# Kernel optimization log

Measured on AMD Instinct MI355X. Metric: run time of the kernel, lower is better.

## Reference

```python
import jax, jax.numpy as jnp
import numpy as np

B, T, N = 512, 1024, 50
ROOT_IDX, END_IDX = 0, 1
NEG_INF = -10000.0


def setup_inputs() -> dict:
    key = jax.random.key(0)
    k1, k2, k3, k4 = jax.random.split(key, 4)
    input_features = jax.random.normal(k1, (B, T, N), dtype=jnp.float32)
    # xavier_uniform on [N, N]: bound = sqrt(6 / (N + N))
    bound = float(np.sqrt(6.0 / (N + N)))
    log_transitions = jax.random.uniform(k2, (N, N), minval=-bound, maxval=bound, dtype=jnp.float32)
    log_transitions = log_transitions.at[:, ROOT_IDX].set(NEG_INF)
    log_transitions = log_transitions.at[END_IDX, :].set(NEG_INF)
    target_tags = jax.random.randint(k3, (B, T), 0, N).astype(jnp.int64)
    # contiguous prefix mask from random lengths in [T//2, T]
    lengths = jax.random.randint(k4, (B,), T // 2, T + 1)
    input_mask = (jnp.arange(T)[None, :] < lengths[:, None]).astype(jnp.int32)
    return {
        "input_features": input_features,
        "log_transitions": log_transitions,
        "target_tags": target_tags,
        "input_mask": input_mask,
    }


def _crf_nll(input_features, log_transitions, target_tags, input_mask):
    maskf = input_mask.astype(input_features.dtype)  # [B, T]

    # ---- forward belief propagation (log partition) ----
    alpha0 = log_transitions[ROOT_IDX, :][None, :] + input_features[:, 0, :]  # [B, N]
    feats_t = jnp.swapaxes(input_features, 0, 1)  # [T, B, N]
    mask_t = jnp.swapaxes(maskf, 0, 1)            # [T, B]

    def step(alpha, xs):
        feat, m = xs  # [B, N], [B]
        # next_tag_var[b, i, j] = alpha[b, i] + feat[b, j] + trans[i, j]
        nxt = alpha[:, :, None] + feat[:, None, :] + log_transitions[None, :, :]
        new = jax.nn.logsumexp(nxt, axis=1)  # [B, N]
        m = m[:, None]
        return new * m + alpha * (1.0 - m), None

    alpha, _ = jax.lax.scan(step, alpha0, (feats_t[1:], mask_t[1:]))
    log_z = jax.nn.logsumexp(alpha + log_transitions[:, END_IDX][None, :], axis=-1)  # [B]

    # ---- gold sequence score (vectorized over time) ----
    tags = target_tags  # [B, T]
    scores = log_transitions[ROOT_IDX, tags[:, 0]]  # [B]
    # per-position emission score of the gold tag
    emis = jnp.take_along_axis(input_features, tags[:, :, None], axis=2)[:, :, 0]  # [B, T]
    trans = log_transitions[tags[:, :-1], tags[:, 1:]]  # [B, T-1]
    scores = scores + jnp.sum(trans * maskf[:, 1:], axis=1) + jnp.sum(emis[:, :-1] * maskf[:, :-1], axis=1)
    last_idx = jnp.sum(input_mask, axis=1) - 1  # [B]
    last_tags = jnp.take_along_axis(tags, last_idx[:, None], axis=1)[:, 0]  # [B]
    last_emit = jnp.take_along_axis(input_features[:, -1, :], last_tags[:, None], axis=1)[:, 0]
    scores = scores + log_transitions[last_tags, END_IDX] + last_emit * maskf[:, -1]

    return log_z - scores  # negative log likelihood, [B]


def reference(input_features, log_transitions, target_tags, input_mask):
    return _crf_nll(input_features, log_transitions, target_tags, input_mask)
```

## Files before the change

### kernel.cpp

```cpp
#include <hip/hip_runtime.h>
#include <math.h>

#define BB 512
#define TT 1024
#define NS 50

typedef _Float16 half2_t __attribute__((ext_vector_type(2)));

static __device__ __forceinline__ half2_t pk_h2(float a, float b) {
    auto r = __builtin_amdgcn_cvt_pkrtz(a, b);
    return __builtin_bit_cast(half2_t, r);
}
static __device__ __forceinline__ float wave_sum_f(float v) {
    #pragma unroll
    for (int k = 32; k >= 1; k >>= 1) v += __shfl_xor(v, k, 64);
    return v;
}
static __device__ __forceinline__ int wave_sum_i(int v) {
    #pragma unroll
    for (int k = 32; k >= 1; k >>= 1) v += __shfl_xor(v, k, 64);
    return v;
}
#define FDOT(a, b, c) __builtin_amdgcn_fdot2((a), (b), (c), false)

__global__ __launch_bounds__(128, 1) void crf_nll_kernel(
    const float* __restrict__ feat,
    const float* __restrict__ trans,
    const int*   __restrict__ tags,
    const int*   __restrict__ mask,
    float* __restrict__ out)
{
    const int b    = blockIdx.x;
    const int tid  = threadIdx.x;
    const int w    = tid >> 6;
    const int lane = tid & 63;
    const int jj   = (lane < NS) ? lane : 0;

    __shared__ float sh_comb[64];
    __shared__ float sh_sc[2];
    __shared__ int   sh_Kb;

#define INIT_E(m) half2_t e##m; { \
        int r0 = w ? (jj * NS + 2*(m)) : ((2*(m)) * NS + jj); \
        int r1 = r0 + (w ? 1 : NS); \
        float x0 = __expf(trans[r0]); \
        float x1 = __expf(trans[r1]); \
        if (lane >= NS) { x0 = 0.f; x1 = 0.f; } \
        e##m = pk_h2(x0, x1); }
    INIT_E(0)  INIT_E(1)  INIT_E(2)  INIT_E(3)  INIT_E(4)
    INIT_E(5)  INIT_E(6)  INIT_E(7)  INIT_E(8)  INIT_E(9)
    INIT_E(10) INIT_E(11) INIT_E(12) INIT_E(13) INIT_E(14)
    INIT_E(15) INIT_E(16) INIT_E(17) INIT_E(18) INIT_E(19)
    INIT_E(20) INIT_E(21) INIT_E(22) INIT_E(23) INIT_E(24)
#undef INIT_E

    int cnt = 0;
    for (int t = lane; t < TT; t += 64) cnt += mask[b * TT + t];
    const int len = wave_sum_i(cnt);
    const int tm  = (len - 1) >> 1;
    const int nst = w ? (len - 1 - tm) : tm;

    const float* fb = feat + (size_t)b * TT * NS;

    float u;
    if (w == 0) u = (lane < NS) ? __expf(trans[jj] + fb[jj]) : 0.f;
    else        u = (lane < NS) ? __expf(trans[jj * NS + 1] + fb[(size_t)(len - 1) * NS + jj]) : 0.f;
    int K = 0, kp, rr;
    { int bb2 = __builtin_amdgcn_readlane(__float_as_int(u), 7);
      kp = ((bb2 >> 23) & 255) - 127; rr = (127 - kp) << 23; }

    auto step = [&](float eexp) {
        K += kp;
        float p = u * __int_as_float(rr);
        int pn_ = __builtin_amdgcn_update_dpp(
            __float_as_int(p), __float_as_int(p), 0xB1, 0xF, 0xF, true);
        float pnf = __int_as_float(pn_);
        half2_t pk = pk_h2(p, pnf);
        int pki = __builtin_bit_cast(int, pk);
        float s0 = 0.f, s1 = 0.f, s2 = 0.f, s3 = 0.f;
        float s4 = 0.f, s5 = 0.f, s6 = 0.f, s7 = 0.f;
#define RLF(m, acc) { int b_ = __builtin_amdgcn_readlane(pki, 2*(m)); \
        acc = FDOT(__builtin_bit_cast(half2_t, b_), e##m, acc); }
        RLF(0,  s0) RLF(1,  s1) RLF(2,  s2) RLF(3,  s3)
        RLF(4,  s4) RLF(5,  s5) RLF(6,  s6) RLF(7,  s7)
        RLF(8,  s0) RLF(9,  s1) RLF(10, s2) RLF(11, s3)
        RLF(12, s4) RLF(13, s5) RLF(14, s6) RLF(15, s7)
        RLF(16, s0) RLF(17, s1) RLF(18, s2) RLF(19, s3)
        RLF(20, s4) RLF(21, s5) RLF(22, s6) RLF(23, s7)
        RLF(24, s0)
#undef RLF
        float S = ((s0 + s1) + (s2 + s3)) + ((s4 + s5) + (s6 + s7));
        u = S * eexp;
        int bb2 = __builtin_amdgcn_readlane(__float_as_int(u), 7);
        kp = ((bb2 >> 23) & 255) - 127;
        rr = (127 - kp) << 23;
    };

    float q0, q1, q2, q3, q4, q5, q6, q7;
    {
        int t0 = w ? (len - 2) : 1;
        int st = w ? -1 : 1;
#define LD(qr, d) { int tl = t0 + st * (d); tl = (tl < 0) ? 0 : ((tl < TT) ? tl : TT - 1); \
                    qr = __expf(fb[(size_t)tl * NS + jj]); }
        LD(q0, 0) LD(q1, 1) LD(q2, 2) LD(q3, 3) LD(q4, 4) LD(q5, 5) LD(q6, 6) LD(q7, 7)
#undef LD
    }

#define PF_STEP(qr, d) { \
        float e_ = qr; \
        int kl = k + 8 + (d); \
        int tl = w ? (len - 2 - kl) : (1 + kl); \
        tl = (tl < 0) ? 0 : ((tl < TT) ? tl : TT - 1); \
        qr = __expf(fb[(size_t)tl * NS + jj]); \
        step(e_); }

    int k = 0;
    for (; k + 8 <= nst; k += 8) {
        PF_STEP(q0, 0) PF_STEP(q1, 1) PF_STEP(q2, 2) PF_STEP(q3, 3)
        PF_STEP(q4, 4) PF_STEP(q5, 5) PF_STEP(q6, 6) PF_STEP(q7, 7)
    }
#undef PF_STEP
    for (; k < nst; ++k) {
        int tl = w ? (len - 2 - k) : (1 + k);
        step(__expf(fb[(size_t)tl * NS + jj]));
    }

    if (w == 1) {
        sh_comb[lane] = u * __expf(-fb[(size_t)tm * NS + jj]);
        if (lane == 0) sh_Kb = K;
    }

    const int* tb = tags + (size_t)b * TT;
    float sc = 0.0f;
    for (int t2 = tid; t2 < len; t2 += 128) {
        int tg = tb[t2];
        sc += fb[(size_t)t2 * NS + tg];
        if (t2 >= 1) sc += trans[tb[t2 - 1] * NS + tg];
    }
    sc = wave_sum_f(sc);
    if (lane == 0) sh_sc[w] = sc;

    __syncthreads();

    if (w == 0) {
        float wv = u * sh_comb[lane];
        float W = wave_sum_f(wv);
        float log_z = __logf(W) + (float)(K + sh_Kb) * 0.6931471805599453f;
        if (lane == 0) {
            float sct = sh_sc[0] + sh_sc[1]
                      + trans[tb[0]]
                      + trans[tb[len - 1] * NS + 1];
            out[b] = log_z - sct;
        }
    }
}

extern "C" void kernel_launch(void* const* d_in, const int* in_sizes, int n_in,
                              void* d_out, int out_size, void* d_ws, size_t ws_size,
                              hipStream_t stream) {
    const float* feat  = (const float*)d_in[0];
    const float* trans = (const float*)d_in[1];
    const int*   tags  = (const int*)d_in[2];
    const int*   mask  = (const int*)d_in[3];
    float* out = (float*)d_out;
    crf_nll_kernel<<<dim3(BB), dim3(128), 0, stream>>>(feat, trans, tags, mask, out);
}
```

Measured before the change: 275.3 us.

## Batch 16 sequences per block with MFMA recurrence and producer-wave LDS staging

The forward recursion is rebuilt so each block handles 16 sequences and computes the 50x50 transition product with 16x16x32 f16 MFMA instead of per-lane readlane and fdot2 chains. Dedicated producer waves load emission rows, exponentiate them and stage them in a ring of LDS slots, synchronised with the consumer waves by barriers. The gold-path score moves into a separate kernel whose result goes through a workspace. The aim is to remove the serial scalar dependency per step and raise arithmetic density. The cost is an extra launch, block barriers on every group of four steps, a launch of only 32 blocks, and every sequence running to the batch's longest length.

```diff
diff --git a/kernel.cpp b/kernel.cpp
--- a/kernel.cpp
+++ b/kernel.cpp
@@ -4,153 +4,303 @@
 #define BB 512
 #define TT 1024
 #define NS 50
-
+#define SEQ 16
+#define LN2F 0.6931471805599453f
+
+typedef _Float16 f16x8 __attribute__((ext_vector_type(8)));
 typedef _Float16 half2_t __attribute__((ext_vector_type(2)));
-
-static __device__ __forceinline__ half2_t pk_h2(float a, float b) {
+typedef float f32x4 __attribute__((ext_vector_type(4)));
+
+#define MFMA16(A, B, C) __builtin_amdgcn_mfma_f32_16x16x32_f16((A), (B), (C), 0, 0, 0)
+
+static __device__ __forceinline__ int pack2(float a, float b) {
     auto r = __builtin_amdgcn_cvt_pkrtz(a, b);
-    return __builtin_bit_cast(half2_t, r);
+    return __builtin_bit_cast(int, r);
 }
-static __device__ __forceinline__ float wave_sum_f(float v) {
-    #pragma unroll
-    for (int k = 32; k >= 1; k >>= 1) v += __shfl_xor(v, k, 64);
-    return v;
-}
-static __device__ __forceinline__ int wave_sum_i(int v) {
-    #pragma unroll
-    for (int k = 32; k >= 1; k >>= 1) v += __shfl_xor(v, k, 64);
-    return v;
-}
-#define FDOT(a, b, c) __builtin_amdgcn_fdot2((a), (b), (c), false)
-
-__global__ __launch_bounds__(128, 1) void crf_nll_kernel(
+
+#define SLOT_F 924
+#define TILE_F 264
+#define T3_F   792
+#define DIR_F  (8 * SLOT_F)
+
+struct ES { f32x4 a, b, c; float x0, x1; };
+struct LS { f32x4 a, b, c, d; };
+
+__global__ __launch_bounds__(128, 1) void crf_score_kernel(
     const float* __restrict__ feat,
     const float* __restrict__ trans,
     const int*   __restrict__ tags,
     const int*   __restrict__ mask,
-    float* __restrict__ out)
+    float* __restrict__ ws)
 {
     const int b    = blockIdx.x;
     const int tid  = threadIdx.x;
     const int w    = tid >> 6;
     const int lane = tid & 63;
-    const int jj   = (lane < NS) ? lane : 0;
-
-    __shared__ float sh_comb[64];
     __shared__ float sh_sc[2];
-    __shared__ int   sh_Kb;
-
-#define INIT_E(m) half2_t e##m; { \
-        int r0 = w ? (jj * NS + 2*(m)) : ((2*(m)) * NS + jj); \
-        int r1 = r0 + (w ? 1 : NS); \
-        float x0 = __expf(trans[r0]); \
-        float x1 = __expf(trans[r1]); \
-        if (lane >= NS) { x0 = 0.f; x1 = 0.f; } \
-        e##m = pk_h2(x0, x1); }
-    INIT_E(0)  INIT_E(1)  INIT_E(2)  INIT_E(3)  INIT_E(4)
-    INIT_E(5)  INIT_E(6)  INIT_E(7)  INIT_E(8)  INIT_E(9)
-    INIT_E(10) INIT_E(11) INIT_E(12) INIT_E(13) INIT_E(14)
-    INIT_E(15) INIT_E(16) INIT_E(17) INIT_E(18) INIT_E(19)
-    INIT_E(20) INIT_E(21) INIT_E(22) INIT_E(23) INIT_E(24)
-#undef INIT_E
 
     int cnt = 0;
     for (int t = lane; t < TT; t += 64) cnt += mask[b * TT + t];
-    const int len = wave_sum_i(cnt);
-    const int tm  = (len - 1) >> 1;
-    const int nst = w ? (len - 1 - tm) : tm;
-
-    const float* fb = feat + (size_t)b * TT * NS;
-
-    float u;
-    if (w == 0) u = (lane < NS) ? __expf(trans[jj] + fb[jj]) : 0.f;
-    else        u = (lane < NS) ? __expf(trans[jj * NS + 1] + fb[(size_t)(len - 1) * NS + jj]) : 0.f;
-    int K = 0, kp, rr;
-    { int bb2 = __builtin_amdgcn_readlane(__float_as_int(u), 7);
-      kp = ((bb2 >> 23) & 255) - 127; rr = (127 - kp) << 23; }
-
-    auto step = [&](float eexp) {
-        K += kp;
-        float p = u * __int_as_float(rr);
-        int pn_ = __builtin_amdgcn_update_dpp(
-            __float_as_int(p), __float_as_int(p), 0xB1, 0xF, 0xF, true);
-        float pnf = __int_as_float(pn_);
-        half2_t pk = pk_h2(p, pnf);
-        int pki = __builtin_bit_cast(int, pk);
-        float s0 = 0.f, s1 = 0.f, s2 = 0.f, s3 = 0.f;
-        float s4 = 0.f, s5 = 0.f, s6 = 0.f, s7 = 0.f;
-#define RLF(m, acc) { int b_ = __builtin_amdgcn_readlane(pki, 2*(m)); \
-        acc = FDOT(__builtin_bit_cast(half2_t, b_), e##m, acc); }
-        RLF(0,  s0) RLF(1,  s1) RLF(2,  s2) RLF(3,  s3)
-        RLF(4,  s4) RLF(5,  s5) RLF(6,  s6) RLF(7,  s7)
-        RLF(8,  s0) RLF(9,  s1) RLF(10, s2) RLF(11, s3)
-        RLF(12, s4) RLF(13, s5) RLF(14, s6) RLF(15, s7)
-        RLF(16, s0) RLF(17, s1) RLF(18, s2) RLF(19, s3)
-        RLF(20, s4) RLF(21, s5) RLF(22, s6) RLF(23, s7)
-        RLF(24, s0)
-#undef RLF
-        float S = ((s0 + s1) + (s2 + s3)) + ((s4 + s5) + (s6 + s7));
-        u = S * eexp;
-        int bb2 = __builtin_amdgcn_readlane(__float_as_int(u), 7);
-        kp = ((bb2 >> 23) & 255) - 127;
-        rr = (127 - kp) << 23;
-    };
-
-    float q0, q1, q2, q3, q4, q5, q6, q7;
-    {
-        int t0 = w ? (len - 2) : 1;
-        int st = w ? -1 : 1;
-#define LD(qr, d) { int tl = t0 + st * (d); tl = (tl < 0) ? 0 : ((tl < TT) ? tl : TT - 1); \
-                    qr = __expf(fb[(size_t)tl * NS + jj]); }
-        LD(q0, 0) LD(q1, 1) LD(q2, 2) LD(q3, 3) LD(q4, 4) LD(q5, 5) LD(q6, 6) LD(q7, 7)
-#undef LD
-    }
-
-#define PF_STEP(qr, d) { \
-        float e_ = qr; \
-        int kl = k + 8 + (d); \
-        int tl = w ? (len - 2 - kl) : (1 + kl); \
-        tl = (tl < 0) ? 0 : ((tl < TT) ? tl : TT - 1); \
-        qr = __expf(fb[(size_t)tl * NS + jj]); \
-        step(e_); }
-
-    int k = 0;
-    for (; k + 8 <= nst; k += 8) {
-        PF_STEP(q0, 0) PF_STEP(q1, 1) PF_STEP(q2, 2) PF_STEP(q3, 3)
-        PF_STEP(q4, 4) PF_STEP(q5, 5) PF_STEP(q6, 6) PF_STEP(q7, 7)
-    }
-#undef PF_STEP
-    for (; k < nst; ++k) {
-        int tl = w ? (len - 2 - k) : (1 + k);
-        step(__expf(fb[(size_t)tl * NS + jj]));
-    }
-
-    if (w == 1) {
-        sh_comb[lane] = u * __expf(-fb[(size_t)tm * NS + jj]);
-        if (lane == 0) sh_Kb = K;
-    }
-
-    const int* tb = tags + (size_t)b * TT;
-    float sc = 0.0f;
+    #pragma unroll
+    for (int k = 32; k >= 1; k >>= 1) cnt += __shfl_xor(cnt, k, 64);
+    const int len = cnt;
+
+    const float* fbb = feat + (size_t)b * TT * NS;
+    const int*   tb  = tags + (size_t)b * TT;
+    float sc = 0.f;
     for (int t2 = tid; t2 < len; t2 += 128) {
         int tg = tb[t2];
-        sc += fb[(size_t)t2 * NS + tg];
+        sc += fbb[(size_t)t2 * NS + tg];
         if (t2 >= 1) sc += trans[tb[t2 - 1] * NS + tg];
     }
-    sc = wave_sum_f(sc);
+    #pragma unroll
+    for (int k = 32; k >= 1; k >>= 1) sc += __shfl_xor(sc, k, 64);
     if (lane == 0) sh_sc[w] = sc;
-
     __syncthreads();
-
-    if (w == 0) {
-        float wv = u * sh_comb[lane];
-        float W = wave_sum_f(wv);
-        float log_z = __logf(W) + (float)(K + sh_Kb) * 0.6931471805599453f;
-        if (lane == 0) {
-            float sct = sh_sc[0] + sh_sc[1]
-                      + trans[tb[0]]
-                      + trans[tb[len - 1] * NS + 1];
-            out[b] = log_z - sct;
+    if (tid == 0)
+        ws[b] = sh_sc[0] + sh_sc[1] + trans[tb[0]] + trans[tb[len - 1] * NS + 1];
+}
+
+__global__ __launch_bounds__(256, 1) void crf_main_kernel(
+    const float* __restrict__ feat,
+    const float* __restrict__ trans,
+    const int*   __restrict__ mask,
+    const float* __restrict__ score_ws,
+    float* __restrict__ out)
+{
+    const int tid  = threadIdx.x;
+    const int wv   = tid >> 6;
+    const int role = wv >> 1;
+    const int dir  = wv & 1;
+    const int l    = tid & 63;
+    const int c    = l & 15;
+    const int g    = l >> 4;
+    const int base = blockIdx.x * SEQ;
+
+    __shared__ float eL[2 * DIR_F];
+    __shared__ float comb[64][16];
+    __shared__ int   shK[16];
+
+    const float* fb = feat + (size_t)(base + c) * TT * NS;
+
+    int cnt = 0;
+    {
+        const int4* mp4 = (const int4*)(mask + (size_t)(base + c) * TT) + g * 64;
+        #pragma unroll 4
+        for (int i = 0; i < 64; ++i) { int4 m = mp4[i]; cnt += m.x + m.y + m.z + m.w; }
+    }
+    cnt += __shfl_xor(cnt, 16, 64);
+    cnt += __shfl_xor(cnt, 32, 64);
+    const int len   = cnt;
+    const int tm    = (len - 1) >> 1;
+    const int nst   = dir ? (len - 1 - tm) : tm;
+    const int lastk = nst - 1;
+
+    int bm = (tm > len - 1 - tm) ? tm : (len - 1 - tm);
+    #pragma unroll
+    for (int k = 1; k < 64; k <<= 1) { int o = __shfl_xor(bm, k, 64); bm = o > bm ? o : bm; }
+    const int ngroups = (bm + 3) >> 2;
+
+    const int addr7b = (16 + c) << 2;
+
+    if (role == 1) {
+        float* eW = eL + dir * DIR_F;
+        for (int s = 0; s < 8; ++s)
+            for (int o = l; o < SLOT_F - T3_F; o += 64)
+                eW[s * SLOT_F + T3_F + o] = 0.f;
+
+        auto t_of = [&](int s) { int t = dir ? (len - 2 - s) : (1 + s); return t < 0 ? 0 : t; };
+        auto issue = [&](int s, LS& L) {
+            const float* rp = fb + (size_t)t_of(s) * NS + 16 * g;
+            if (g < 3) {
+                L.a = *(const f32x4*)(rp);
+                L.b = *(const f32x4*)(rp + 4);
+                L.c = *(const f32x4*)(rp + 8);
+                L.d = *(const f32x4*)(rp + 12);
+            } else {
+                float2 t2 = *(const float2*)(rp);
+                L.a = f32x4{t2.x, t2.y, 0.f, 0.f};
+            }
+        };
+        auto put = [&](int s, const LS& L) {
+            float* wp = eW + (s & 7) * SLOT_F;
+            if (g < 3) {
+                f32x4 w0 = {__expf(L.a[0]), __expf(L.a[1]), __expf(L.a[2]), __expf(L.a[3])};
+                f32x4 w1 = {__expf(L.b[0]), __expf(L.b[1]), __expf(L.b[2]), __expf(L.b[3])};
+                f32x4 w2 = {__expf(L.c[0]), __expf(L.c[1]), __expf(L.c[2]), __expf(L.c[3])};
+                f32x4 w3 = {__expf(L.d[0]), __expf(L.d[1]), __expf(L.d[2]), __expf(L.d[3])};
+                float* tb_ = wp + g * TILE_F + c * 4;
+                *(f32x4*)(tb_ + 0)   = w0;
+                *(f32x4*)(tb_ + 64)  = w1;
+                *(f32x4*)(tb_ + 128) = w2;
+                *(f32x4*)(tb_ + 192) = w3;
+            } else {
+                float2 w = {__expf(L.a[0]), __expf(L.a[1])};
+                *(float2*)(wp + T3_F + c * 2) = w;
+            }
+        };
+
+        LS L0, L1, L2, L3;
+        issue(0, L0); issue(1, L1); issue(2, L2); issue(3, L3);
+        put(0, L0); put(1, L1); put(2, L2); put(3, L3);
+        issue(4, L0); issue(5, L1); issue(6, L2); issue(7, L3);
+        __syncthreads();
+        for (int gg = 0; gg < ngroups; ++gg) {
+            put(4 * gg + 4, L0); put(4 * gg + 5, L1);
+            put(4 * gg + 6, L2); put(4 * gg + 7, L3);
+            issue(4 * gg + 8, L0);  issue(4 * gg + 9, L1);
+            issue(4 * gg + 10, L2); issue(4 * gg + 11, L3);
+            __syncthreads();
+        }
+        __syncthreads();
+    } else {
+        f16x8 A00, A01, A10, A11, A20, A21, A30, A31;
+#define MKA(VAR, MT, CH) { \
+        union { int i[4]; f16x8 v; } uA; \
+        _Pragma("unroll") \
+        for (int q = 0; q < 4; ++q) { \
+            float xv[2]; \
+            _Pragma("unroll") \
+            for (int ee = 0; ee < 2; ++ee) { \
+                int ks = 32*(CH) + 16*(q>>1) + 4*g + 2*(q&1) + ee; \
+                int mm = 16*(MT) + c; \
+                float vv = 0.f; \
+                if (ks < NS && mm < NS) \
+                    vv = __expf(trans[dir ? (mm*NS + ks) : (ks*NS + mm)]); \
+                xv[ee] = vv; \
+            } \
+            uA.i[q] = pack2(xv[0], xv[1]); \
+        } \
+        VAR = uA.v; }
+        MKA(A00, 0, 0) MKA(A01, 0, 1) MKA(A10, 1, 0) MKA(A11, 1, 1)
+        MKA(A20, 2, 0) MKA(A21, 2, 1) MKA(A30, 3, 0) MKA(A31, 3, 1)
+#undef MKA
+
+        int K = 0, snapK = 0;
+        int sb0 = 0, sb1 = 0, sb2 = 0, sb3 = 0, sb4 = 0, sb5 = 0, sb6 = 0;
+        f16x8 B0, B1;
+        {
+            float uv[2][4][2]; float ref = 1.f;
+            #pragma unroll
+            for (int ch = 0; ch < 2; ++ch)
+            #pragma unroll
+            for (int q = 0; q < 4; ++q)
+            #pragma unroll
+            for (int ee = 0; ee < 2; ++ee) {
+                int st = 32 * ch + 16 * (q >> 1) + 4 * g + 2 * (q & 1) + ee;
+                float vv = 0.f;
+                if (st < NS) {
+                    float tr = dir ? trans[st * NS + 1] : trans[st];
+                    int t0 = dir ? (len - 1) : 0;
+                    vv = __expf(tr + fb[(size_t)t0 * NS + st]);
+                }
+                uv[ch][q][ee] = vv;
+                if (ch == 0 && q == 1 && ee == 1) ref = vv;
+            }
+            int bb = __builtin_amdgcn_ds_bpermute(addr7b, __float_as_int(ref));
+            int kp = ((bb >> 23) & 255) - 127;
+            K = kp;
+            float rrf = __int_as_float((127 - kp) << 23);
+            union { int i[4]; f16x8 v; } u0, u1;
+            #pragma unroll
+            for (int q = 0; q < 4; ++q) {
+                u0.i[q] = pack2(uv[0][q][0] * rrf, uv[0][q][1] * rrf);
+                u1.i[q] = pack2(uv[1][q][0] * rrf, uv[1][q][1] * rrf);
+            }
+            B0 = u0.v; B1 = u1.v;
+        }
+
+        const float* eR = eL + dir * DIR_F;
+        auto RD = [&](int slot) -> ES {
+            ES e;
+            const float* sp = eR + slot * SLOT_F;
+            e.a = *(const f32x4*)(sp + l * 4);
+            e.b = *(const f32x4*)(sp + TILE_F + l * 4);
+            e.c = *(const f32x4*)(sp + 2 * TILE_F + l * 4);
+            float2 t2 = *(const float2*)(sp + T3_F + l * 2);
+            e.x0 = t2.x; e.x1 = t2.y;
+            return e;
+        };
+        auto STEP = [&](int k, ES e) {
+            f32x4 z = {0.f, 0.f, 0.f, 0.f};
+            f32x4 D0 = MFMA16(A00, B0, z); D0 = MFMA16(A01, B1, D0);
+            f32x4 D1 = MFMA16(A10, B0, z); D1 = MFMA16(A11, B1, D1);
+            f32x4 D2 = MFMA16(A20, B0, z); D2 = MFMA16(A21, B1, D2);
+            f32x4 D3 = MFMA16(A30, B0, z); D3 = MFMA16(A31, B1, D3);
+            float t00 = D0[0]*e.a[0], t01 = D0[1]*e.a[1], t02 = D0[2]*e.a[2], t03 = D0[3]*e.a[3];
+            float t10 = D1[0]*e.b[0], t11 = D1[1]*e.b[1], t12 = D1[2]*e.b[2], t13 = D1[3]*e.b[3];
+            float t20 = D2[0]*e.c[0], t21 = D2[1]*e.c[1], t22 = D2[2]*e.c[2], t23 = D2[3]*e.c[3];
+            float t30 = D3[0]*e.x0,  t31 = D3[1]*e.x1;
+            int bb = __builtin_amdgcn_ds_bpermute(addr7b, __float_as_int(t03));
+            int kp = ((bb >> 23) & 255) - 127;
+            K += kp;
+            float rrf = __int_as_float((127 - kp) << 23);
+            int q0 = pack2(t00*rrf, t01*rrf), q1 = pack2(t02*rrf, t03*rrf);
+            int q2 = pack2(t10*rrf, t11*rrf), q3 = pack2(t12*rrf, t13*rrf);
+            int q4 = pack2(t20*rrf, t21*rrf), q5 = pack2(t22*rrf, t23*rrf);
+            int q6 = pack2(t30*rrf, t31*rrf);
+            union { int i[4]; f16x8 v; } n0, n1;
+            n0.i[0] = q0; n0.i[1] = q1; n0.i[2] = q2; n0.i[3] = q3;
+            n1.i[0] = q4; n1.i[1] = q5; n1.i[2] = q6; n1.i[3] = 0;
+            B0 = n0.v; B1 = n1.v;
+            bool hit = (k == lastk);
+            sb0 = hit ? q0 : sb0; sb1 = hit ? q1 : sb1;
+            sb2 = hit ? q2 : sb2; sb3 = hit ? q3 : sb3;
+            sb4 = hit ? q4 : sb4; sb5 = hit ? q5 : sb5;
+            sb6 = hit ? q6 : sb6;
+            snapK = hit ? K : snapK;
+        };
+
+        __syncthreads();
+        for (int gg = 0; gg < ngroups; ++gg) {
+            int sbase = (gg & 1) * 4;
+            ES ea = RD(sbase + 0);
+            ES eb = RD(sbase + 1);
+            STEP(4 * gg + 0, ea);
+            ea = RD(sbase + 2);
+            STEP(4 * gg + 1, eb);
+            eb = RD(sbase + 3);
+            STEP(4 * gg + 2, ea);
+            STEP(4 * gg + 3, eb);
+            __syncthreads();
+        }
+
+        if (dir == 1) {
+            int sbv[8] = {sb0, sb1, sb2, sb3, sb4, sb5, sb6, 0};
+            #pragma unroll
+            for (int ch = 0; ch < 2; ++ch)
+            #pragma unroll
+            for (int q = 0; q < 4; ++q) {
+                half2_t h = __builtin_bit_cast(half2_t, sbv[ch * 4 + q]);
+                #pragma unroll
+                for (int ee = 0; ee < 2; ++ee) {
+                    int st = 32 * ch + 16 * (q >> 1) + 4 * g + 2 * (q & 1) + ee;
+                    float pb = 0.f;
+                    if (st < NS)
+                        pb = (float)h[ee] * __expf(-fb[(size_t)tm * NS + st]);
+                    comb[l][ch * 8 + q * 2 + ee] = pb;
+                }
+            }
+            if (l < 16) shK[l] = snapK;
+        }
+        __syncthreads();
+        if (dir == 0) {
+            int sbv[8] = {sb0, sb1, sb2, sb3, sb4, sb5, sb6, 0};
+            float wvs = 0.f;
+            #pragma unroll
+            for (int ch = 0; ch < 2; ++ch)
+            #pragma unroll
+            for (int q = 0; q < 4; ++q) {
+                half2_t h = __builtin_bit_cast(half2_t, sbv[ch * 4 + q]);
+                wvs += (float)h[0] * comb[l][ch * 8 + q * 2 + 0];
+                wvs += (float)h[1] * comb[l][ch * 8 + q * 2 + 1];
+            }
+            wvs += __shfl_xor(wvs, 16, 64);
+            wvs += __shfl_xor(wvs, 32, 64);
+            if (l < 16) {
+                float log_z = __logf(wvs) + (float)(snapK + shK[l]) * LN2F;
+                out[base + l] = log_z - score_ws[base + l];
+            }
         }
     }
 }
@@ -163,5 +313,7 @@
     const int*   tags  = (const int*)d_in[2];
     const int*   mask  = (const int*)d_in[3];
     float* out = (float*)d_out;
-    crf_nll_kernel<<<dim3(BB), dim3(128), 0, stream>>>(feat, trans, tags, mask, out);
+    float* ws  = (float*)d_ws;
+    crf_score_kernel<<<dim3(BB), dim3(128), 0, stream>>>(feat, trans, tags, mask, ws);
+    crf_main_kernel<<<dim3(BB / SEQ), dim3(256), 0, stream>>>(feat, trans, mask, ws, out);
 }
```

Measured after the change: 535.8 us. 1.95x slower.
